# Kernel optimization log

Measured on AMD Instinct MI355X. Metric: run time of the kernel, lower is better.

Reference implementation:

```python
import jax, jax.numpy as jnp
import numpy as np

D_MODEL = 512
STATE_DIM = 32
ACTION_DIM = 8
D_STATE = 16
D_CONV = 4
EXPAND = 2
D_INNER = EXPAND * D_MODEL          # 1024
DT_RANK = (D_MODEL + 15) // 16      # 32
BATCH, SEQLEN = 16, 1024


def silu(v):
    return v * jax.nn.sigmoid(v)


def setup_inputs() -> dict:
    key = jax.random.key(0)
    ks = jax.random.split(key, 16)
    s = 0.02
    inp = {
        "x": jax.random.normal(ks[0], (BATCH, SEQLEN, STATE_DIM), jnp.float32),
        "W_emb": jax.random.normal(ks[1], (D_MODEL, STATE_DIM), jnp.float32) * s,
        "b_emb": jnp.zeros((D_MODEL,), jnp.float32),
        "W_in": jax.random.normal(ks[2], (2 * D_INNER, D_MODEL), jnp.float32) * s,
        "conv_w": jax.random.normal(ks[3], (D_INNER, 1, D_CONV), jnp.float32) * s,
        "conv_b": jnp.zeros((D_INNER,), jnp.float32),
        "W_xproj": jax.random.normal(ks[4], (DT_RANK + 2 * D_STATE, D_INNER), jnp.float32) * s,
        "W_dt": jax.random.normal(ks[5], (D_INNER, DT_RANK), jnp.float32) * s,
        "b_dt": jnp.full((D_INNER,), -4.6, jnp.float32),  # ~softplus^-1(0.01)
        "A_log": jnp.log(jnp.broadcast_to(
            jnp.arange(1, D_STATE + 1, dtype=jnp.float32), (D_INNER, D_STATE))),
        "Dskip": jnp.ones((D_INNER,), jnp.float32),
        "W_out": jax.random.normal(ks[6], (D_MODEL, D_INNER), jnp.float32) * s,
        "W_critic": jax.random.normal(ks[7], (1, D_MODEL), jnp.float32) * s,
        "b_critic": jnp.zeros((1,), jnp.float32),
        "W_amean": jax.random.normal(ks[8], (ACTION_DIM, D_MODEL), jnp.float32) * 0.01,  # orthogonal gain=0.01 proxy
        "b_amean": jnp.zeros((ACTION_DIM,), jnp.float32),
        "W_astd": jax.random.normal(ks[9], (ACTION_DIM, D_MODEL), jnp.float32) * s,
        "b_astd": jnp.zeros((ACTION_DIM,), jnp.float32),
    }
    return inp


def _forward(x, W_emb, b_emb, W_in, conv_w, conv_b, W_xproj, W_dt, b_dt,
             A_log, Dskip, W_out, W_critic, b_critic, W_amean, b_amean,
             W_astd, b_astd):
    Bsz = x.shape[0]
    embed = silu(x @ W_emb.T + b_emb)                      # (B,L,D)
    xz = embed @ W_in.T                                     # (B,L,2*Di)
    xu, z = jnp.split(xz, 2, axis=-1)
    # depthwise causal conv1d over time
    xc = jnp.transpose(xu, (0, 2, 1))                       # (B,Di,L)
    conv = jax.lax.conv_general_dilated(
        xc, conv_w, window_strides=(1,), padding=[(D_CONV - 1, 0)],
        dimension_numbers=("NCH", "OIH", "NCH"),
        feature_group_count=D_INNER) + conv_b[None, :, None]
    u = silu(jnp.transpose(conv, (0, 2, 1)))                # (B,L,Di)
    x_dbl = u @ W_xproj.T                                   # (B,L,dt_rank+2N)
    dt, Bm, Cm = jnp.split(x_dbl, [DT_RANK, DT_RANK + D_STATE], axis=-1)
    delta = jax.nn.softplus(dt @ W_dt.T + b_dt)             # (B,L,Di)
    A = -jnp.exp(A_log)                                     # (Di,N)

    # selective scan, time-major
    dlt = jnp.transpose(delta, (1, 0, 2))
    ut = jnp.transpose(u, (1, 0, 2))
    Bt = jnp.transpose(Bm, (1, 0, 2))
    Ct = jnp.transpose(Cm, (1, 0, 2))

    def step(h, inps):
        d_t, u_t, b_t, c_t = inps                           # (B,Di),(B,Di),(B,N),(B,N)
        dA = jnp.exp(d_t[..., None] * A)                    # (B,Di,N)
        h = dA * h + (d_t * u_t)[..., None] * b_t[:, None, :]
        y = jnp.einsum("bdn,bn->bd", h, c_t)
        return h, y

    h0 = jnp.zeros((Bsz, D_INNER, D_STATE), embed.dtype)
    _, ys = jax.lax.scan(step, h0, (dlt, ut, Bt, Ct))       # ys: (L,B,Di)
    y = jnp.transpose(ys, (1, 0, 2)) + u * Dskip
    y = y * silu(z)
    m = y @ W_out.T                                         # (B,L,D)

    # layer_norm (no affine) + silu, last token
    mu = m.mean(-1, keepdims=True)
    var = ((m - mu) ** 2).mean(-1, keepdims=True)
    n = silu((m - mu) / jnp.sqrt(var + 1e-5))[:, -1]        # (B,D)

    value = (n @ W_critic.T + b_critic).squeeze(-1)         # (B,)
    action_mean = n @ W_amean.T + b_amean                   # (B,A)
    log_std = jnp.clip(n @ W_astd.T + b_astd, -1.0, 1.0)
    action_sd = jnp.exp(log_std)
    return action_mean, action_sd, value


def reference(x, W_emb, b_emb, W_in, conv_w, conv_b, W_xproj, W_dt, b_dt,
              A_log, Dskip, W_out, W_critic, b_critic, W_amean, b_amean,
              W_astd, b_astd):
    # Returns the Normal distribution parameters (mean, std) and value,
    # matching torch's (Normal(mean, sd), value).
    return _forward(x, W_emb, b_emb, W_in, conv_w, conv_b, W_xproj, W_dt,
                    b_dt, A_log, Dskip, W_out, W_critic, b_critic,
                    W_amean, b_amean, W_astd, b_astd)
```

## Files before the change

### kernel.cpp

```cpp
#include <hip/hip_runtime.h>
#include <hip/hip_bf16.h>
#include <math.h>

#define B_   16
#define L_   1024
#define DM   512
#define DI   1024
#define NST  16
#define DTR  32
#define ML   (B_*L_)
#define SEGT 64
#define NSEG (L_/SEGT)

typedef __hip_bfloat16 bf16;
typedef __attribute__((ext_vector_type(8))) short short8;
typedef __attribute__((ext_vector_type(4))) float f32x4;

__device__ __forceinline__ float bf2f(unsigned short u) {
  union { unsigned int i; float f; } v; v.i = ((unsigned int)u) << 16; return v.f;
}
__device__ __forceinline__ unsigned short f2bfbits(float f) {
  bf16 h = __float2bfloat16(f);
  return *(unsigned short*)&h;
}
__device__ __forceinline__ float sigmoidf_(float v) { return 1.f/(1.f+__expf(-v)); }
__device__ __forceinline__ float ldf(const void* p, size_t i, int fl) {
  return fl ? bf2f(((const unsigned short*)p)[i]) : ((const float*)p)[i];
}
__device__ __forceinline__ void gload16(const void* g, void* l) {
  __builtin_amdgcn_global_load_lds(
      (const __attribute__((address_space(1))) void*)g,
      (__attribute__((address_space(3))) void*)l, 16, 0, 0);
}
__device__ __forceinline__ short8 ds_read128(unsigned addr) {
  short8 r;
  asm volatile("ds_read_b128 %0, %1" : "=v"(r) : "v"(addr));
  return r;
}

template<typename T> struct LD8;
template<> struct LD8<unsigned short> {
  static __device__ __forceinline__ short8 ld(const void* p, size_t i) {
    return *(const short8*)((const unsigned short*)p + i);
  }
  static __device__ __forceinline__ float lds(const void* p, size_t i) {
    return bf2f(((const unsigned short*)p)[i]);
  }
};
template<> struct LD8<float> {
  static __device__ __forceinline__ short8 ld(const void* p, size_t i) {
    const float* fp = (const float*)p + i;
    float4 f0 = *(const float4*)fp;
    float4 f1 = *(const float4*)(fp + 4);
    short8 v;
    v[0]=(short)f2bfbits(f0.x); v[1]=(short)f2bfbits(f0.y);
    v[2]=(short)f2bfbits(f0.z); v[3]=(short)f2bfbits(f0.w);
    v[4]=(short)f2bfbits(f1.x); v[5]=(short)f2bfbits(f1.y);
    v[6]=(short)f2bfbits(f1.z); v[7]=(short)f2bfbits(f1.w);
    return v;
  }
  static __device__ __forceinline__ float lds(const void* p, size_t i) {
    return ((const float*)p)[i];
  }
};

__global__ void detect_k(const unsigned int* __restrict__ x,
                         const void* __restrict__ A_log, int* __restrict__ flag) {
  int tid = threadIdx.x;
  int cnt = 0;
  for (int i = tid; i < 256; i += 64) {
    float a = fabsf(bf2f((unsigned short)(x[i] & 0xffffu)));
    if (a > 1e-3f && a < 10.f) cnt++;
  }
  for (int off = 32; off >= 1; off >>= 1) cnt += __shfl_xor(cnt, off);
  int fl = (cnt >= 128) ? 1 : 0;
  int n = tid & 15;
  int row = (tid < 16) ? 0 : (tid < 32 ? 512 : 1023);
  float al = ldf(A_log, (size_t)row*NST + n, fl);
  int ok = (fabsf(al - __logf((float)(n+1))) <= 0.02f) ? 1 : 0;
  for (int off = 32; off >= 1; off >>= 1) ok &= __shfl_xor(ok, off);
  if (tid == 0) { flag[0] = fl; flag[1] = ok; flag[2] = 1; }
}

__global__ __launch_bounds__(256) void convert_k(
    const void* __restrict__ x, const void* __restrict__ W_emb,
    const void* __restrict__ b_emb, const void* __restrict__ W_in,
    const void* __restrict__ W_xproj,
    unsigned short* __restrict__ xbf, unsigned short* __restrict__ webf,
    unsigned short* __restrict__ bebf, unsigned short* __restrict__ wibf,
    unsigned short* __restrict__ wxbf, const int* __restrict__ flag)
{
  const int fl = *flag;
  size_t t = (size_t)blockIdx.x*256 + threadIdx.x;
  const size_t n0 = (size_t)ML*32/8;
  const size_t n1 = (size_t)DM*32/8;
  const size_t n2 = DM/8;
  const size_t n3 = (size_t)DI*DM/8;
  const size_t n4 = (size_t)64*DI/8;
  const void* src; unsigned short* dst; size_t e;
  if      (t < n0)             { src = x;       dst = xbf;  e = t; }
  else if (t < n0+n1)          { src = W_emb;   dst = webf; e = t-n0; }
  else if (t < n0+n1+n2)       { src = b_emb;   dst = bebf; e = t-n0-n1; }
  else if (t < n0+n1+n2+n3)    { src = W_in;    dst = wibf; e = t-n0-n1-n2; }
  else if (t < n0+n1+n2+n3+n4) { src = W_xproj; dst = wxbf; e = t-n0-n1-n2-n3; }
  else return;
  size_t i = e*8;
  if (fl) *(short8*)&dst[i] = *(const short8*)((const unsigned short*)src + i);
  else    *(short8*)&dst[i] = LD8<float>::ld(src, i);
}

__global__ __launch_bounds__(512, 2) void gemm256_k(
    const unsigned short* __restrict__ A, const unsigned short* __restrict__ W,
    unsigned short* __restrict__ C, int K, int lda, int ldb, int ldc,
    const void* __restrict__ conv_w, const void* __restrict__ conv_b,
    unsigned short* __restrict__ xubnd, const int* __restrict__ flag)
{
  if (!flag[2]) return;
  __shared__ unsigned short smem[2][2][256*64];
  const int tid = threadIdx.x;
  const int lane = tid & 63;
  const int wv = tid >> 6;
  const int wr = wv >> 2;
  const int wc = wv & 3;
  const int m0 = blockIdx.x * 256;
  const int n0 = blockIdx.y * 256;
  const int lr = lane & 15, lg = lane >> 4;
  const int drow = lane >> 3;
  const int scol = ((lane & 7) ^ drow) * 8;
  const int NKT = K >> 6;
  const unsigned lds0 = (unsigned)(unsigned long long)
      (__attribute__((address_space(3))) void*)&smem[0][0][0];

  f32x4 acc[8][4];
  #pragma unroll
  for (int i = 0; i < 8; ++i)
    #pragma unroll
    for (int j = 0; j < 4; ++j) acc[i][j] = (f32x4){0.f, 0.f, 0.f, 0.f};

  auto stage = [&](int buf, int kt) {
    #pragma unroll
    for (int q = 0; q < 4; ++q) {
      int rb = (wv*4 + q) * 8;
      gload16(A + (size_t)(m0 + rb + drow)*lda + kt*64 + scol, &smem[buf][0][rb*64]);
    }
    #pragma unroll
    for (int q = 0; q < 4; ++q) {
      int rb = (wv*4 + q) * 8;
      gload16(W + (size_t)(n0 + rb + drow)*ldb + kt*64 + scol, &smem[buf][1][rb*64]);
    }
  };

  stage(0, 0);
  stage(1, 1);
  for (int kt = 0; kt < NKT; ++kt) {
    int buf = kt & 1;
    if (kt + 1 < NKT) asm volatile("s_waitcnt vmcnt(8)" ::: "memory");
    else              asm volatile("s_waitcnt vmcnt(0)" ::: "memory");
    __builtin_amdgcn_s_barrier();
    __builtin_amdgcn_sched_barrier(0);
    const unsigned aBase = lds0 + (unsigned)(buf*2 + 0)*(256*64*2);
    const unsigned bBase = lds0 + (unsigned)(buf*2 + 1)*(256*64*2);
    #pragma unroll
    for (int kk = 0; kk < 64; kk += 32) {
      const int ukk = (((kk >> 3) + lg) ^ (lr & 7)) * 8;
      short8 af[8], bfr[4];
      #pragma unroll
      for (int i = 0; i < 8; ++i)
        af[i] = ds_read128(aBase + (unsigned)(((wr*128 + i*16 + lr)*64 + ukk)*2));
      #pragma unroll
      for (int j = 0; j < 4; ++j)
        bfr[j] = ds_read128(bBase + (unsigned)(((wc*64 + j*16 + lr)*64 + ukk)*2));
      asm volatile("s_waitcnt lgkmcnt(0)" ::: "memory");
      __builtin_amdgcn_sched_barrier(0);
      __builtin_amdgcn_s_setprio(1);
      #pragma unroll
      for (int i = 0; i < 8; ++i)
        #pragma unroll
        for (int j = 0; j < 4; ++j)
          acc[i][j] = __builtin_amdgcn_mfma_f32_16x16x32_bf16(af[i], bfr[j], acc[i][j], 0, 0, 0);
      __builtin_amdgcn_s_setprio(0);
    }
    __builtin_amdgcn_s_barrier();
    __builtin_amdgcn_sched_barrier(0);
    if (kt + 2 < NKT) stage(buf, kt + 2);
  }

  unsigned short* cs = (unsigned short*)smem;
  #pragma unroll
  for (int j = 0; j < 4; ++j) {
    int c = wc*64 + j*16 + lr;
    #pragma unroll
    for (int i = 0; i < 8; ++i) {
      int rbase = wr*128 + i*16 + lg*4;
      #pragma unroll
      for (int r = 0; r < 4; ++r)
        cs[(rbase + r)*256 + c] = f2bfbits(acc[i][j][r]);
    }
  }
  __syncthreads();
  const int fl = flag[0];
  const int t0loc = m0 & (L_ - 1);
  const int colb = (tid & 31) * 8;
  const int rowbase = (tid >> 5) * 16;
  float wt[8][4], bt[8];
  #pragma unroll
  for (int e = 0; e < 8; ++e) {
    int d = n0 + colb + e;
    #pragma unroll
    for (int q = 0; q < 4; ++q) wt[e][q] = ldf(conv_w, (size_t)d*4 + q, fl);
    bt[e] = ldf(conv_b, d, fl);
  }
  const int tileIdx = blockIdx.x*4 + blockIdx.y;
  short8 zer;
  #pragma unroll
  for (int e = 0; e < 8; ++e) zer[e] = 0;
  short8 c1 = (rowbase >= 1) ? *(const short8*)&cs[(rowbase-1)*256 + colb] : zer;
  short8 c2 = (rowbase >= 2) ? *(const short8*)&cs[(rowbase-2)*256 + colb] : zer;
  short8 c3 = (rowbase >= 3) ? *(const short8*)&cs[(rowbase-3)*256 + colb] : zer;
  #pragma unroll
  for (int k = 0; k < 16; ++k) {
    int row = rowbase + k;
    short8 c0 = *(const short8*)&cs[row*256 + colb];
    if (row < 3 || row >= 253) {
      int rm = (row < 3) ? row : row - 250;
      *(short8*)&xubnd[((size_t)tileIdx*6 + rm)*256 + colb] = c0;
    }
    if (!(row < 3 && t0loc != 0)) {
      short8 out;
      #pragma unroll
      for (int e = 0; e < 8; ++e) {
        float ca  = bf2f((unsigned short)c0[e]);
        float am1 = bf2f((unsigned short)c1[e]);
        float am2 = bf2f((unsigned short)c2[e]);
        float am3 = bf2f((unsigned short)c3[e]);
        float va = wt[e][0]*am3 + wt[e][1]*am2 + wt[e][2]*am1 + wt[e][3]*ca + bt[e];
        va = va * sigmoidf_(va);
        out[e] = (short)f2bfbits(va);
      }
      *(short8*)&C[(size_t)(m0 + row)*ldc + n0 + colb] = out;
    }
    c3 = c2; c2 = c1; c1 = c0;
  }
}

__global__ __launch_bounds__(256) void convfix_k(
    const unsigned short* __restrict__ xubnd,
    const void* __restrict__ conv_w, const void* __restrict__ conv_b,
    unsigned short* __restrict__ u, const int* __restrict__ flag)
{
  int tile = blockIdx.x;
  int r = blockIdx.y;
  int mt = tile >> 2, nt = tile & 3;
  int m0 = mt*256, n0 = nt*256;
  if ((m0 & (L_ - 1)) == 0) return;
  int col = threadIdx.x;
  int d = n0 + col;
  int fl = flag[0];
  float vin[4];
  #pragma unroll
  for (int q = 0; q < 4; ++q) {
    int trow = r - 3 + q;
    int stile, srm;
    if (trow < 0) { stile = tile - 4; srm = 6 + trow; }
    else          { stile = tile;     srm = trow; }
    vin[q] = bf2f(xubnd[((size_t)stile*6 + srm)*256 + col]);
  }
  float w0 = ldf(conv_w, (size_t)d*4 + 0, fl);
  float w1 = ldf(conv_w, (size_t)d*4 + 1, fl);
  float w2 = ldf(conv_w, (size_t)d*4 + 2, fl);
  float w3 = ldf(conv_w, (size_t)d*4 + 3, fl);
  float bb = ldf(conv_b, d, fl);
  float va = w0*vin[0] + w1*vin[1] + w2*vin[2] + w3*vin[3] + bb;
  va = va * sigmoidf_(va);
  u[(size_t)(m0 + r)*DI + d] = f2bfbits(va);
}


template<int BM, int BN, int BK>
__device__ __forceinline__ void mfma_body_dma(
    const unsigned short* __restrict__ A, const unsigned short* __restrict__ W,
    const unsigned short* __restrict__ bias, void* __restrict__ Cv,
    int K, int lda, int ldb, int ldc, int mode, size_t csplit)
{
  extern __shared__ unsigned short smem[];
  unsigned short* As = smem;
  unsigned short* Bs = smem + BM*BK;
  constexpr int MIM = (BM == 64) ? 4 : ((BN == 128) ? 4 : 2);
  constexpr int MIN = (BM == 64) ? 2 : 4;
  constexpr int RPI = 1024/(2*BK);
  constexpr int LPR = 64/RPI;
  const int tid = threadIdx.x;
  const int m0 = blockIdx.x * BM;
  const int n0 = blockIdx.y * BN;
  const int kbase = blockIdx.z * K;
  const int lane = tid & 63;
  const int wv = tid >> 6;
  const int wm = (BM == 64) ? 0 : ((BN == 128) ? (wv >> 1) * 64 : wv * 32);
  const int wn = (BM == 64) ? wv * 32 : ((BN == 128) ? (wv & 1) * 64 : 0);
  const int lr = lane & 15, lg = lane >> 4;
  const int drow = lane / LPR;
  const int dcol = (lane % LPR) * 8;

  f32x4 acc[MIM][MIN];
  #pragma unroll
  for (int i = 0; i < MIM; ++i)
    #pragma unroll
    for (int j = 0; j < MIN; ++j) acc[i][j] = (f32x4){0.f, 0.f, 0.f, 0.f};

  for (int k0 = 0; k0 < K; k0 += BK) {
    __syncthreads();
    #pragma unroll
    for (int q = 0; q < BM/RPI/4; ++q) {
      int rb = (wv*(BM/RPI/4) + q) * RPI;
      gload16(A + (size_t)(m0 + rb + drow)*lda + kbase + k0 + dcol, &As[rb*BK]);
    }
    #pragma unroll
    for (int q = 0; q < BN/RPI/4; ++q) {
      int rb = (wv*(BN/RPI/4) + q) * RPI;
      gload16(W + (size_t)(n0 + rb + drow)*ldb + kbase + k0 + dcol, &Bs[rb*BK]);
    }
    __syncthreads();
    #pragma unroll
    for (int kk = 0; kk < BK; kk += 32) {
      short8 af[MIM], bfr[MIN];
      #pragma unroll
      for (int i = 0; i < MIM; ++i)
        af[i] = *(const short8*)&As[(wm + i*16 + lr)*BK + kk + lg*8];
      #pragma unroll
      for (int j = 0; j < MIN; ++j)
        bfr[j] = *(const short8*)&Bs[(wn + j*16 + lr)*BK + kk + lg*8];
      #pragma unroll
      for (int i = 0; i < MIM; ++i)
        #pragma unroll
        for (int j = 0; j < MIN; ++j)
          acc[i][j] = __builtin_amdgcn_mfma_f32_16x16x32_bf16(af[i], bfr[j], acc[i][j], 0, 0, 0);
    }
  }

  size_t cz = (size_t)blockIdx.z * csplit;
  #pragma unroll
  for (int j = 0; j < MIN; ++j) {
    int gn = n0 + wn + j*16 + lr;
    float bv = (mode == 1) ? bf2f(bias[gn]) : 0.f;
    #pragma unroll
    for (int i = 0; i < MIM; ++i) {
      #pragma unroll
      for (int r = 0; r < 4; ++r) {
        int gm = m0 + wm + i*16 + lg*4 + r;
        float v = acc[i][j][r];
        if (mode == 1) {
          v += bv; v = v * sigmoidf_(v);
          ((unsigned short*)Cv)[cz + (size_t)gm*ldc + gn] = f2bfbits(v);
        } else if (mode == 3) {
          ((unsigned short*)Cv)[cz + (size_t)gm*ldc + gn] = f2bfbits(v);
        } else {
          ((float*)Cv)[cz + (size_t)gm*ldc + gn] = v;
        }
      }
    }
  }
}

template<typename TA, typename TW, int BM, int BN>
__device__ __forceinline__ void mfma_body(
    const void* __restrict__ Av, const void* __restrict__ Wv,
    const void* __restrict__ biasv, void* __restrict__ Cv,
    int K, int lda, int ldb, int ldc, int mode, size_t csplit)
{
  extern __shared__ unsigned short smem[];
  unsigned short* As = smem;
  unsigned short* Bs = smem + BM*40;
  constexpr int MIM = (BM == 64) ? 4 : ((BN == 128) ? 4 : 2);
  constexpr int MIN = (BM == 64) ? 2 : 4;
  const int tid = threadIdx.x;
  const int m0 = blockIdx.x * BM;
  const int n0 = blockIdx.y * BN;
  const int kbase = blockIdx.z * K;
  const int lane = tid & 63;
  const int wv = tid >> 6;
  const int wm = (BM == 64) ? 0 : ((BN == 128) ? (wv >> 1) * 64 : wv * 32);
  const int wn = (BM == 64) ? wv * 32 : ((BN == 128) ? (wv & 1) * 64 : 0);
  const int lr = lane & 15, lg = lane >> 4;

  f32x4 acc[MIM][MIN];
  #pragma unroll
  for (int i = 0; i < MIM; ++i)
    #pragma unroll
    for (int j = 0; j < MIN; ++j) acc[i][j] = (f32x4){0.f, 0.f, 0.f, 0.f};

  for (int k0 = 0; k0 < K; k0 += 32) {
    short8 ra[BM/64], rb[BN/64];
    #pragma unroll
    for (int r = 0; r < BM/64; ++r) {
      int chunk = tid + r*256;
      int row = chunk >> 2, sub = (chunk & 3) * 8;
      ra[r] = LD8<TA>::ld(Av, (size_t)(m0 + row)*lda + kbase + k0 + sub);
    }
    #pragma unroll
    for (int r = 0; r < BN/64; ++r) {
      int chunk = tid + r*256;
      int row = chunk >> 2, sub = (chunk & 3) * 8;
      rb[r] = LD8<TW>::ld(Wv, (size_t)(n0 + row)*ldb + kbase + k0 + sub);
    }
    __syncthreads();
    #pragma unroll
    for (int r = 0; r < BM/64; ++r) {
      int chunk = tid + r*256;
      int row = chunk >> 2, sub = (chunk & 3) * 8;
      *(short8*)&As[row*40 + sub] = ra[r];
    }
    #pragma unroll
    for (int r = 0; r < BN/64; ++r) {
      int chunk = tid + r*256;
      int row = chunk >> 2, sub = (chunk & 3) * 8;
      *(short8*)&Bs[row*40 + sub] = rb[r];
    }
    __syncthreads();
    short8 af[MIM], bfr[MIN];
    #pragma unroll
    for (int i = 0; i < MIM; ++i)
      af[i] = *(const short8*)&As[(wm + i*16 + lr)*40 + lg*8];
    #pragma unroll
    for (int j = 0; j < MIN; ++j)
      bfr[j] = *(const short8*)&Bs[(wn + j*16 + lr)*40 + lg*8];
    #pragma unroll
    for (int i = 0; i < MIM; ++i)
      #pragma unroll
      for (int j = 0; j < MIN; ++j)
        acc[i][j] = __builtin_amdgcn_mfma_f32_16x16x32_bf16(af[i], bfr[j], acc[i][j], 0, 0, 0);
  }

  size_t cz = (size_t)blockIdx.z * csplit;
  #pragma unroll
  for (int j = 0; j < MIN; ++j) {
    int gn = n0 + wn + j*16 + lr;
    float bv = (mode == 1) ? LD8<TW>::lds(biasv, gn) : 0.f;
    #pragma unroll
    for (int i = 0; i < MIM; ++i) {
      #pragma unroll
      for (int r = 0; r < 4; ++r) {
        int gm = m0 + wm + i*16 + lg*4 + r;
        float v = acc[i][j][r];
        if (mode == 1) {
          v += bv; v = v * sigmoidf_(v);
          ((unsigned short*)Cv)[cz + (size_t)gm*ldc + gn] = f2bfbits(v);
        } else if (mode == 3) {
          ((unsigned short*)Cv)[cz + (size_t)gm*ldc + gn] = f2bfbits(v);
        } else {
          ((float*)Cv)[cz + (size_t)gm*ldc + gn] = v;
        }
      }
    }
  }
}

template<int BM, int BN, int BK>
__global__ __launch_bounds__(256) void gemm_a16_k(const void* A, const void* W,
    const void* bias, void* C, int K, int lda, int ldb, int ldc, int mode,
    size_t csplit, const int* __restrict__ flag)
{
  if (*flag) mfma_body_dma<BM, BN, BK>((const unsigned short*)A, (const unsigned short*)W,
                                       (const unsigned short*)bias, C, K, lda, ldb, ldc, mode, csplit);
  else       mfma_body<unsigned short, float, BM, BN>(A, W, bias, C, K, lda, ldb, ldc, mode, csplit);
}

__global__ __launch_bounds__(256) void dt_gemm_k(
    const float* __restrict__ xd, const void* __restrict__ W_dt,
    const void* __restrict__ b_dt, unsigned short* __restrict__ delta,
    const int* __restrict__ flag)
{
  __shared__ unsigned short As[128*40];
  __shared__ unsigned short Bs[128*40];
  const int tid = threadIdx.x;
  const int m0 = blockIdx.x * 128;
  const int n0 = blockIdx.y * 128;
  const int fl = *flag;
  const int row = tid >> 1, half = (tid & 1) * 16;
  {
    size_t g = (size_t)(m0 + row)*64 + half;
    const float* p0 = xd + g;
    const float* p1 = xd + (size_t)ML*64 + g;
    short8 v0, v1;
    #pragma unroll
    for (int q = 0; q < 8; q += 4) {
      float4 a4 = *(const float4*)(p0 + q);
      float4 b4 = *(const float4*)(p1 + q);
      v0[q+0] = (short)f2bfbits(a4.x + b4.x);
      v0[q+1] = (short)f2bfbits(a4.y + b4.y);
      v0[q+2] = (short)f2bfbits(a4.z + b4.z);
      v0[q+3] = (short)f2bfbits(a4.w + b4.w);
    }
    #pragma unroll
    for (int q = 0; q < 8; q += 4) {
      float4 a4 = *(const float4*)(p0 + 8 + q);
      float4 b4 = *(const float4*)(p1 + 8 + q);
      v1[q+0] = (short)f2bfbits(a4.x + b4.x);
      v1[q+1] = (short)f2bfbits(a4.y + b4.y);
      v1[q+2] = (short)f2bfbits(a4.z + b4.z);
      v1[q+3] = (short)f2bfbits(a4.w + b4.w);
    }
    *(short8*)&As[row*40 + half] = v0;
    *(short8*)&As[row*40 + half + 8] = v1;
  }
  {
    *(short8*)&Bs[row*40 + half]     = fl ? LD8<unsigned short>::ld(W_dt, (size_t)(n0+row)*DTR + half)
                                          : LD8<float>::ld(W_dt, (size_t)(n0+row)*DTR + half);
    *(short8*)&Bs[row*40 + half + 8] = fl ? LD8<unsigned short>::ld(W_dt, (size_t)(n0+row)*DTR + half + 8)
                                          : LD8<float>::ld(W_dt, (size_t)(n0+row)*DTR + half + 8);
  }
  __syncthreads();
  const int lane = tid & 63;
  const int wv = tid >> 6;
  const int wm = (wv >> 1) * 64, wn = (wv & 1) * 64;
  const int lr = lane & 15, lg = lane >> 4;
  f32x4 acc[4][4];
  #pragma unroll
  for (int i = 0; i < 4; ++i)
    #pragma unroll
    for (int j = 0; j < 4; ++j) acc[i][j] = (f32x4){0.f, 0.f, 0.f, 0.f};
  short8 af[4], bfr[4];
  #pragma unroll
  for (int i = 0; i < 4; ++i)
    af[i] = *(const short8*)&As[(wm + i*16 + lr)*40 + lg*8];
  #pragma unroll
  for (int j = 0; j < 4; ++j)
    bfr[j] = *(const short8*)&Bs[(wn + j*16 + lr)*40 + lg*8];
  #pragma unroll
  for (int i = 0; i < 4; ++i)
    #pragma unroll
    for (int j = 0; j < 4; ++j)
      acc[i][j] = __builtin_amdgcn_mfma_f32_16x16x32_bf16(af[i], bfr[j], acc[i][j], 0, 0, 0);
  #pragma unroll
  for (int j = 0; j < 4; ++j) {
    int gn = n0 + wn + j*16 + lr;
    float bv = ldf(b_dt, gn, fl);
    #pragma unroll
    for (int i = 0; i < 4; ++i) {
      #pragma unroll
      for (int r = 0; r < 4; ++r) {
        int gm = m0 + wm + i*16 + lg*4 + r;
        float v = acc[i][j][r] + bv;
        v = (v > 20.f) ? v : __logf(1.f + __expf(v));
        delta[(size_t)gm*DI + gn] = f2bfbits(v);
      }
    }
  }
}

__global__ __launch_bounds__(256) void zlast2_k(const unsigned short* __restrict__ embed,
    const void* __restrict__ W_in, float* __restrict__ z_last, const int* __restrict__ flag)
{
  int b = blockIdx.x;
  int j0 = blockIdx.y * 64;
  int tid = threadIdx.x;
  __shared__ float e[DM];
  for (int i = tid; i < DM; i += 256)
    e[i] = bf2f(embed[(size_t)(b*L_ + L_-1)*DM + i]);
  __syncthreads();
  int fl = *flag;
  int wid = tid >> 6, lane = tid & 63;
  for (int jj = wid; jj < 64; jj += 4) {
    int j = j0 + jj;
    float p = 0.f;
    int k = lane * 8;
    if (fl) {
      const unsigned short* w = (const unsigned short*)W_in + (size_t)(DI + j)*DM + k;
      short8 v = *(const short8*)w;
      #pragma unroll
      for (int q = 0; q < 8; ++q) p += e[k+q]*bf2f((unsigned short)v[q]);
    } else {
      const float* w = (const float*)W_in + (size_t)(DI + j)*DM + k;
      float4 v0 = *(const float4*)w;
      float4 v1 = *(const float4*)(w + 4);
      p = e[k]*v0.x + e[k+1]*v0.y + e[k+2]*v0.z + e[k+3]*v0.w
        + e[k+4]*v1.x + e[k+5]*v1.y + e[k+6]*v1.z + e[k+7]*v1.w;
    }
    for (int off = 32; off >= 1; off >>= 1) p += __shfl_xor(p, off);
    if (lane == 0) z_last[b*DI + j] = p;
  }
}

__global__ __launch_bounds__(256) void scan4_k(
    const unsigned short* __restrict__ delta, const unsigned short* __restrict__ u,
    const float* __restrict__ xd, const void* __restrict__ A_log,
    unsigned int* __restrict__ ps, const int* __restrict__ flag)
{
  const int b = blockIdx.x;
  const int d0 = blockIdx.y * 256;
  const int seg = blockIdx.z;
  const int t0 = seg * SEGT;
  const int tid = threadIdx.x;
  const int d = d0 + tid;
  const int fl = flag[0];
  const int fast = flag[1];
  __shared__ float sB[SEGT*16];
  #pragma unroll
  for (int i = 0; i < SEGT*16/256; ++i) {
    int idx = tid + i*256;
    int row = idx >> 4, n = idx & 15;
    size_t g = (size_t)(b*L_ + t0 + row)*64 + 32 + n;
    sB[idx] = xd[g] + xd[(size_t)ML*64 + g];
  }
  float h[16];
  #pragma unroll
  for (int n = 0; n < 16; ++n) h[n] = 0.f;
  float sdt = 0.f;
  const unsigned short* dp = delta + (size_t)(b*L_ + t0)*DI + d;
  const unsigned short* up = u + (size_t)(b*L_ + t0)*DI + d;
  __syncthreads();
  if (fast) {
    unsigned short nd = dp[0], nu = up[0];
    for (int t = 0; t < SEGT; ++t) {
      float dt = bf2f(nd), ut = bf2f(nu);
      if (t < SEGT-1) { nd = dp[(size_t)(t+1)*DI]; nu = up[(size_t)(t+1)*DI]; }
      float g = dt * ut;
      sdt += dt;
      const float* Br = &sB[t*16];
      float e1 = __expf(-dt);
      float e = e1;
      h[0] = e*h[0] + g*Br[0];
      #pragma unroll
      for (int n = 1; n < 16; ++n) {
        e *= e1;
        h[n] = e*h[n] + g*Br[n];
      }
    }
    float E1 = __expf(-sdt);
    float P = 1.f;
    #pragma unroll
    for (int n = 0; n < 16; ++n) {
      P *= E1;
      ps[(((size_t)seg*16 + b)*16 + n)*DI + d] =
          ((unsigned int)f2bfbits(h[n]) << 16) | f2bfbits(P);
    }
  } else {
    float a[16];
    #pragma unroll
    for (int n = 0; n < 16; ++n)
      a[n] = -__expf(ldf(A_log, (size_t)d*NST + n, fl));
    unsigned short nd = dp[0], nu = up[0];
    for (int t = 0; t < SEGT; ++t) {
      float dt = bf2f(nd), ut = bf2f(nu);
      if (t < SEGT-1) { nd = dp[(size_t)(t+1)*DI]; nu = up[(size_t)(t+1)*DI]; }
      float g = dt * ut;
      sdt += dt;
      const float* Br = &sB[t*16];
      #pragma unroll
      for (int n = 0; n < 16; ++n)
        h[n] = __expf(dt*a[n])*h[n] + g*Br[n];
    }
    #pragma unroll
    for (int n = 0; n < 16; ++n)
      ps[(((size_t)seg*16 + b)*16 + n)*DI + d] =
          ((unsigned int)f2bfbits(h[n]) << 16) | f2bfbits(__expf(a[n]*sdt));
  }
}

__global__ __launch_bounds__(256) void combine4_k(const unsigned int* __restrict__ ps,
    const float* __restrict__ xd, float* __restrict__ ypart)
{
  int b = blockIdx.x;
  int d = blockIdx.y * 256 + threadIdx.x;
  int n0 = blockIdx.z * 4;
  float h[4] = {0.f, 0.f, 0.f, 0.f};
  for (int s = 0; s < NSEG; ++s) {
    #pragma unroll
    for (int q = 0; q < 4; ++q) {
      unsigned int v = ps[(((size_t)s*16 + b)*16 + n0 + q)*DI + d];
      h[q] = bf2f((unsigned short)v)*h[q] + bf2f((unsigned short)(v >> 16));
    }
  }
  float y = 0.f;
  #pragma unroll
  for (int q = 0; q < 4; ++q) {
    size_t gl = (size_t)(b*L_ + L_-1)*64 + 48 + n0 + q;
    float cn = xd[gl] + xd[(size_t)ML*64 + gl];
    y += h[q]*cn;
  }
  ypart[((size_t)blockIdx.z*16 + b)*DI + d] = y;
}

__global__ __launch_bounds__(256) void mdot_k(const float* __restrict__ ypart,
    const unsigned short* __restrict__ u, const float* __restrict__ z_last,
    const void* __restrict__ Dskip, const void* __restrict__ W_out,
    float* __restrict__ m_out, const int* __restrict__ flag)
{
  int b = blockIdx.x;
  int r0 = blockIdx.y * 64;
  int tid = threadIdx.x;
  const int fl = *flag;
  __shared__ float yz[DI];
  for (int i = tid; i < DI; i += 256) {
    float ys = ypart[(size_t)b*DI + i] + ypart[(size_t)(16+b)*DI + i]
             + ypart[(size_t)(32+b)*DI + i] + ypart[(size_t)(48+b)*DI + i]
             + bf2f(u[(size_t)(b*L_ + L_-1)*DI + i]) * ldf(Dskip, i, fl);
    float z = z_last[b*DI + i];
    yz[i] = ys * (z * sigmoidf_(z));
  }
  __syncthreads();
  int wid = tid >> 6, lane = tid & 63;
  int k = lane * 8;
  for (int rr = wid; rr < 64; rr += 4) {
    int row = r0 + rr;
    float p = 0.f;
    if (fl) {
      const unsigned short* w = (const unsigned short*)W_out + (size_t)row*DI;
      short8 v0 = *(const short8*)(w + k);
      short8 v1 = *(const short8*)(w + 512 + k);
      #pragma unroll
      for (int q = 0; q < 8; ++q)
        p += yz[k+q]*bf2f((unsigned short)v0[q]) + yz[512+k+q]*bf2f((unsigned short)v1[q]);
    } else {
      const float* w = (const float*)W_out + (size_t)row*DI;
      float4 a0 = *(const float4*)(w + k),      a1 = *(const float4*)(w + k + 4);
      float4 b0 = *(const float4*)(w + 512 + k), b1 = *(const float4*)(w + 512 + k + 4);
      p = yz[k]*a0.x + yz[k+1]*a0.y + yz[k+2]*a0.z + yz[k+3]*a0.w
        + yz[k+4]*a1.x + yz[k+5]*a1.y + yz[k+6]*a1.z + yz[k+7]*a1.w
        + yz[512+k]*b0.x + yz[512+k+1]*b0.y + yz[512+k+2]*b0.z + yz[512+k+3]*b0.w
        + yz[512+k+4]*b1.x + yz[512+k+5]*b1.y + yz[512+k+6]*b1.z + yz[512+k+7]*b1.w;
    }
    for (int off = 32; off >= 1; off >>= 1) p += __shfl_xor(p, off);
    if (lane == 0) m_out[b*DM + row] = p;
  }
}

__global__ __launch_bounds__(512) void head2_k(const float* __restrict__ m_in,
    const void* __restrict__ W_critic, const void* __restrict__ b_critic,
    const void* __restrict__ W_amean, const void* __restrict__ b_amean,
    const void* __restrict__ W_astd, const void* __restrict__ b_astd,
    void* __restrict__ out, const int* __restrict__ flag)
{
  __shared__ float nb[DM];
  __shared__ float w1[8], w2[8];
  const int fl = *flag;
  int b = blockIdx.x;
  int tid = threadIdx.x;
  float m = m_in[b*DM + tid];
  float s1 = m, s2 = m*m;
  for (int off = 32; off >= 1; off >>= 1) { s1 += __shfl_xor(s1, off); s2 += __shfl_xor(s2, off); }
  int wid = tid >> 6, lane = tid & 63;
  if (lane == 0) { w1[wid] = s1; w2[wid] = s2; }
  __syncthreads();
  float t1 = 0.f, t2 = 0.f;
  for (int i = 0; i < 8; ++i) { t1 += w1[i]; t2 += w2[i]; }
  float mu  = t1 * (1.f/DM);
  float var = t2 * (1.f/DM) - mu*mu;
  float v = (m - mu) * rsqrtf(var + 1e-5f);
  nb[tid] = v * sigmoidf_(v);
  __syncthreads();
  for (int o = wid; o < 17; o += 8) {
    const void* w; size_t woff; float bias;
    if (o < 8)       { w = W_amean; woff = (size_t)o*DM;     bias = ldf(b_amean, o, fl); }
    else if (o < 16) { w = W_astd;  woff = (size_t)(o-8)*DM; bias = ldf(b_astd, o-8, fl); }
    else             { w = W_critic; woff = 0;               bias = ldf(b_critic, 0, fl); }
    float p = 0.f;
    for (int j = lane; j < DM; j += 64) p += nb[j] * ldf(w, woff + j, fl);
    for (int off = 32; off >= 1; off >>= 1) p += __shfl_xor(p, off);
    if (lane == 0) {
      float r = p + bias;
      int idx; float val;
      if (o < 8)       { idx = b*8 + o;           val = r; }
      else if (o < 16) { float ls = fminf(1.f, fmaxf(-1.f, r));
                         idx = 128 + b*8 + (o-8); val = expf(ls); }
      else             { idx = 256 + b;           val = r; }
      if (fl) ((bf16*)out)[idx] = __float2bfloat16(val);
      else    ((float*)out)[idx] = val;
    }
  }
}

extern "C" void kernel_launch(void* const* d_in, const int* in_sizes, int n_in,
                              void* d_out, int out_size, void* d_ws, size_t ws_size,
                              hipStream_t stream)
{
  const void* x        = d_in[0];
  const void* W_emb    = d_in[1];
  const void* b_emb    = d_in[2];
  const void* W_in     = d_in[3];
  const void* conv_w   = d_in[4];
  const void* conv_b   = d_in[5];
  const void* W_xproj  = d_in[6];
  const void* W_dt     = d_in[7];
  const void* b_dt     = d_in[8];
  const void* A_log    = d_in[9];
  const void* Dskip    = d_in[10];
  const void* W_out    = d_in[11];
  const void* W_critic = d_in[12];
  const void* b_critic = d_in[13];
  const void* W_amean  = d_in[14];
  const void* b_amean  = d_in[15];
  const void* W_astd   = d_in[16];
  const void* b_astd   = d_in[17];

  char* ws = (char*)d_ws;
  unsigned short* embed_bf = (unsigned short*)ws; ws += (size_t)ML*DM*2;
  unsigned short* dlt_b = (unsigned short*)ws; ws += (size_t)ML*DI*2;
  unsigned short* u_b   = (unsigned short*)ws; ws += (size_t)ML*DI*2;
  float* xdbl2 = (float*)ws; ws += (size_t)2*ML*64*4;
  unsigned int* psbuf = (unsigned int*)ws; ws += (size_t)NSEG*B_*NST*DI*4;
  float* ypart = (float*)ws; ws += (size_t)4*B_*DI*4;
  float* zlast = (float*)ws; ws += (size_t)B_*DI*4;
  float* mbuf  = (float*)ws; ws += (size_t)B_*DM*4;
  int*   flag  = (int*)ws;   ws += 64;
  unsigned short* xbf  = (unsigned short*)ws; ws += (size_t)ML*32*2;
  unsigned short* webf = (unsigned short*)ws; ws += (size_t)DM*32*2;
  unsigned short* bebf = (unsigned short*)ws; ws += (size_t)DM*2;
  unsigned short* wibf = (unsigned short*)ws; ws += (size_t)DI*DM*2;
  unsigned short* wxbf = (unsigned short*)ws; ws += (size_t)64*DI*2;
  unsigned short* xubnd = (unsigned short*)ws; ws += (size_t)256*6*256*2;
  const int* flagBF = flag + 2;

  detect_k<<<1, 64, 0, stream>>>((const unsigned int*)x, A_log, flag);
  convert_k<<<553, 256, 0, stream>>>(x, W_emb, b_emb, W_in, W_xproj,
                                     xbf, webf, bebf, wibf, wxbf, flag);
  gemm_a16_k<128, 128, 32><<<dim3(ML/128, DM/128), 256, 256*40*2, stream>>>(
      xbf, webf, bebf, embed_bf, 32, 32, 32, DM, 1, 0, flagBF);
  gemm256_k<<<dim3(ML/256, DI/256), 512, 0, stream>>>(
      embed_bf, wibf, u_b, DM, DM, DM, DI, conv_w, conv_b, xubnd, flag);
  convfix_k<<<dim3(256, 3), 256, 0, stream>>>(xubnd, conv_w, conv_b, u_b, flag);
  zlast2_k<<<dim3(16, 16), 256, 0, stream>>>(embed_bf, W_in, zlast, flag);
  gemm_a16_k<128, 64, 64><<<dim3(ML/128, 1, 2), 256, 24576, stream>>>(
      u_b, wxbf, nullptr, xdbl2, 512, DI, DI, 64, 0, (size_t)ML*64, flagBF);
  dt_gemm_k<<<dim3(ML/128, DI/128), 256, 0, stream>>>(
      xdbl2, W_dt, b_dt, dlt_b, flag);
  scan4_k<<<dim3(B_, 4, NSEG), 256, 0, stream>>>(
      dlt_b, u_b, xdbl2, A_log, psbuf, flag);
  combine4_k<<<dim3(B_, 4, 4), 256, 0, stream>>>(psbuf, xdbl2, ypart);
  mdot_k<<<dim3(16, 8), 256, 0, stream>>>(ypart, u_b, zlast, Dskip, W_out, mbuf, flag);
  head2_k<<<16, 512, 0, stream>>>(mbuf, W_critic, b_critic,
                                  W_amean, b_amean, W_astd, b_astd, (void*)d_out, flag);
}
```

Baseline: 251.0 us.

## Fuse dt projection GEMM and softplus into the segmented scan kernel

Removes the separate dt_gemm kernel and computes delta for each scan segment inside the scan kernel. The kernel uses one MFMA per 16x16 tile from the dt-rank slice of xdbl and a bf16 copy of W_dt, applies softplus, and stores the result in shared memory. This avoids writing and re-reading a B*L*DI bf16 delta tensor in global memory and saves one launch. In exchange, the scan kernel uses more shared memory, does extra prologue work per block, and takes on a convert_k pass that converts W_dt to bf16.

```diff
diff --git a/kernel.cpp b/kernel.cpp
--- a/kernel.cpp
+++ b/kernel.cpp
@@ -85,10 +85,11 @@
 __global__ __launch_bounds__(256) void convert_k(
     const void* __restrict__ x, const void* __restrict__ W_emb,
     const void* __restrict__ b_emb, const void* __restrict__ W_in,
-    const void* __restrict__ W_xproj,
+    const void* __restrict__ W_xproj, const void* __restrict__ W_dt,
     unsigned short* __restrict__ xbf, unsigned short* __restrict__ webf,
     unsigned short* __restrict__ bebf, unsigned short* __restrict__ wibf,
-    unsigned short* __restrict__ wxbf, const int* __restrict__ flag)
+    unsigned short* __restrict__ wxbf, unsigned short* __restrict__ wdtbf,
+    const int* __restrict__ flag)
 {
   const int fl = *flag;
   size_t t = (size_t)blockIdx.x*256 + threadIdx.x;
@@ -97,12 +98,14 @@
   const size_t n2 = DM/8;
   const size_t n3 = (size_t)DI*DM/8;
   const size_t n4 = (size_t)64*DI/8;
+  const size_t n5 = (size_t)DI*DTR/8;
   const void* src; unsigned short* dst; size_t e;
-  if      (t < n0)             { src = x;       dst = xbf;  e = t; }
-  else if (t < n0+n1)          { src = W_emb;   dst = webf; e = t-n0; }
-  else if (t < n0+n1+n2)       { src = b_emb;   dst = bebf; e = t-n0-n1; }
-  else if (t < n0+n1+n2+n3)    { src = W_in;    dst = wibf; e = t-n0-n1-n2; }
-  else if (t < n0+n1+n2+n3+n4) { src = W_xproj; dst = wxbf; e = t-n0-n1-n2-n3; }
+  if      (t < n0)                { src = x;       dst = xbf;   e = t; }
+  else if (t < n0+n1)             { src = W_emb;   dst = webf;  e = t-n0; }
+  else if (t < n0+n1+n2)          { src = b_emb;   dst = bebf;  e = t-n0-n1; }
+  else if (t < n0+n1+n2+n3)       { src = W_in;    dst = wibf;  e = t-n0-n1-n2; }
+  else if (t < n0+n1+n2+n3+n4)    { src = W_xproj; dst = wxbf;  e = t-n0-n1-n2-n3; }
+  else if (t < n0+n1+n2+n3+n4+n5) { src = W_dt;    dst = wdtbf; e = t-n0-n1-n2-n3-n4; }
   else return;
   size_t i = e*8;
   if (fl) *(short8*)&dst[i] = *(const short8*)((const unsigned short*)src + i);
@@ -464,89 +467,6 @@
   else       mfma_body<unsigned short, float, BM, BN>(A, W, bias, C, K, lda, ldb, ldc, mode, csplit);
 }
 
-__global__ __launch_bounds__(256) void dt_gemm_k(
-    const float* __restrict__ xd, const void* __restrict__ W_dt,
-    const void* __restrict__ b_dt, unsigned short* __restrict__ delta,
-    const int* __restrict__ flag)
-{
-  __shared__ unsigned short As[128*40];
-  __shared__ unsigned short Bs[128*40];
-  const int tid = threadIdx.x;
-  const int m0 = blockIdx.x * 128;
-  const int n0 = blockIdx.y * 128;
-  const int fl = *flag;
-  const int row = tid >> 1, half = (tid & 1) * 16;
-  {
-    size_t g = (size_t)(m0 + row)*64 + half;
-    const float* p0 = xd + g;
-    const float* p1 = xd + (size_t)ML*64 + g;
-    short8 v0, v1;
-    #pragma unroll
-    for (int q = 0; q < 8; q += 4) {
-      float4 a4 = *(const float4*)(p0 + q);
-      float4 b4 = *(const float4*)(p1 + q);
-      v0[q+0] = (short)f2bfbits(a4.x + b4.x);
-      v0[q+1] = (short)f2bfbits(a4.y + b4.y);
-      v0[q+2] = (short)f2bfbits(a4.z + b4.z);
-      v0[q+3] = (short)f2bfbits(a4.w + b4.w);
-    }
-    #pragma unroll
-    for (int q = 0; q < 8; q += 4) {
-      float4 a4 = *(const float4*)(p0 + 8 + q);
-      float4 b4 = *(const float4*)(p1 + 8 + q);
-      v1[q+0] = (short)f2bfbits(a4.x + b4.x);
-      v1[q+1] = (short)f2bfbits(a4.y + b4.y);
-      v1[q+2] = (short)f2bfbits(a4.z + b4.z);
-      v1[q+3] = (short)f2bfbits(a4.w + b4.w);
-    }
-    *(short8*)&As[row*40 + half] = v0;
-    *(short8*)&As[row*40 + half + 8] = v1;
-  }
-  {
-    *(short8*)&Bs[row*40 + half]     = fl ? LD8<unsigned short>::ld(W_dt, (size_t)(n0+row)*DTR + half)
-                                          : LD8<float>::ld(W_dt, (size_t)(n0+row)*DTR + half);
-    *(short8*)&Bs[row*40 + half + 8] = fl ? LD8<unsigned short>::ld(W_dt, (size_t)(n0+row)*DTR + half + 8)
-                                          : LD8<float>::ld(W_dt, (size_t)(n0+row)*DTR + half + 8);
-  }
-  __syncthreads();
-  const int lane = tid & 63;
-  const int wv = tid >> 6;
-  const int wm = (wv >> 1) * 64, wn = (wv & 1) * 64;
-  const int lr = lane & 15, lg = lane >> 4;
-  f32x4 acc[4][4];
-  #pragma unroll
-  for (int i = 0; i < 4; ++i)
-    #pragma unroll
-    for (int j = 0; j < 4; ++j) acc[i][j] = (f32x4){0.f, 0.f, 0.f, 0.f};
-  short8 af[4], bfr[4];
-  #pragma unroll
-  for (int i = 0; i < 4; ++i)
-    af[i] = *(const short8*)&As[(wm + i*16 + lr)*40 + lg*8];
-  #pragma unroll
-  for (int j = 0; j < 4; ++j)
-    bfr[j] = *(const short8*)&Bs[(wn + j*16 + lr)*40 + lg*8];
-  #pragma unroll
-  for (int i = 0; i < 4; ++i)
-    #pragma unroll
-    for (int j = 0; j < 4; ++j)
-      acc[i][j] = __builtin_amdgcn_mfma_f32_16x16x32_bf16(af[i], bfr[j], acc[i][j], 0, 0, 0);
-  #pragma unroll
-  for (int j = 0; j < 4; ++j) {
-    int gn = n0 + wn + j*16 + lr;
-    float bv = ldf(b_dt, gn, fl);
-    #pragma unroll
-    for (int i = 0; i < 4; ++i) {
-      #pragma unroll
-      for (int r = 0; r < 4; ++r) {
-        int gm = m0 + wm + i*16 + lg*4 + r;
-        float v = acc[i][j][r] + bv;
-        v = (v > 20.f) ? v : __logf(1.f + __expf(v));
-        delta[(size_t)gm*DI + gn] = f2bfbits(v);
-      }
-    }
-  }
-}
-
 __global__ __launch_bounds__(256) void zlast2_k(const unsigned short* __restrict__ embed,
     const void* __restrict__ W_in, float* __restrict__ z_last, const int* __restrict__ flag)
 {
@@ -580,10 +500,11 @@
   }
 }
 
-__global__ __launch_bounds__(256) void scan4_k(
-    const unsigned short* __restrict__ delta, const unsigned short* __restrict__ u,
-    const float* __restrict__ xd, const void* __restrict__ A_log,
-    unsigned int* __restrict__ ps, const int* __restrict__ flag)
+__global__ __launch_bounds__(256) void scan6_k(
+    const unsigned short* __restrict__ u, const float* __restrict__ xd,
+    const unsigned short* __restrict__ wdtbf, const void* __restrict__ b_dt,
+    const void* __restrict__ A_log, unsigned int* __restrict__ ps,
+    const int* __restrict__ flag)
 {
   const int b = blockIdx.x;
   const int d0 = blockIdx.y * 256;
@@ -594,6 +515,8 @@
   const int fl = flag[0];
   const int fast = flag[1];
   __shared__ float sB[SEGT*16];
+  __shared__ unsigned short sDT[SEGT*32];
+  __shared__ unsigned short sDelta[SEGT*256];
   #pragma unroll
   for (int i = 0; i < SEGT*16/256; ++i) {
     int idx = tid + i*256;
@@ -601,18 +524,43 @@
     size_t g = (size_t)(b*L_ + t0 + row)*64 + 32 + n;
     sB[idx] = xd[g] + xd[(size_t)ML*64 + g];
   }
+  #pragma unroll
+  for (int i = 0; i < SEGT*32/256; ++i) {
+    int idx = tid + i*256;
+    size_t g = (size_t)(b*L_ + t0 + (idx >> 5))*64 + (idx & 31);
+    sDT[idx] = f2bfbits(xd[g] + xd[(size_t)ML*64 + g]);
+  }
+  __syncthreads();
+  {
+    const int lane = tid & 63;
+    const int wv4 = tid >> 6;
+    const int lr = lane & 15, lg = lane >> 4;
+    short8 af = *(const short8*)&sDT[(wv4*16 + lr)*32 + lg*8];
+    #pragma unroll
+    for (int j = 0; j < 16; ++j) {
+      short8 bfr = *(const short8*)&wdtbf[(size_t)(d0 + j*16 + lr)*DTR + lg*8];
+      f32x4 a4 = (f32x4){0.f, 0.f, 0.f, 0.f};
+      a4 = __builtin_amdgcn_mfma_f32_16x16x32_bf16(af, bfr, a4, 0, 0, 0);
+      float bv = ldf(b_dt, d0 + j*16 + lr, fl);
+      #pragma unroll
+      for (int r = 0; r < 4; ++r) {
+        float v = a4[r] + bv;
+        v = (v > 20.f) ? v : __logf(1.f + __expf(v));
+        sDelta[(wv4*16 + lg*4 + r)*256 + j*16 + lr] = f2bfbits(v);
+      }
+    }
+  }
   float h[16];
   #pragma unroll
   for (int n = 0; n < 16; ++n) h[n] = 0.f;
   float sdt = 0.f;
-  const unsigned short* dp = delta + (size_t)(b*L_ + t0)*DI + d;
   const unsigned short* up = u + (size_t)(b*L_ + t0)*DI + d;
   __syncthreads();
   if (fast) {
-    unsigned short nd = dp[0], nu = up[0];
+    unsigned short nu = up[0];
     for (int t = 0; t < SEGT; ++t) {
-      float dt = bf2f(nd), ut = bf2f(nu);
-      if (t < SEGT-1) { nd = dp[(size_t)(t+1)*DI]; nu = up[(size_t)(t+1)*DI]; }
+      float dt = bf2f(sDelta[t*256 + tid]), ut = bf2f(nu);
+      if (t < SEGT-1) nu = up[(size_t)(t+1)*DI];
       float g = dt * ut;
       sdt += dt;
       const float* Br = &sB[t*16];
@@ -638,10 +586,10 @@
     #pragma unroll
     for (int n = 0; n < 16; ++n)
       a[n] = -__expf(ldf(A_log, (size_t)d*NST + n, fl));
-    unsigned short nd = dp[0], nu = up[0];
+    unsigned short nu = up[0];
     for (int t = 0; t < SEGT; ++t) {
-      float dt = bf2f(nd), ut = bf2f(nu);
-      if (t < SEGT-1) { nd = dp[(size_t)(t+1)*DI]; nu = up[(size_t)(t+1)*DI]; }
+      float dt = bf2f(sDelta[t*256 + tid]), ut = bf2f(nu);
+      if (t < SEGT-1) nu = up[(size_t)(t+1)*DI];
       float g = dt * ut;
       sdt += dt;
       const float* Br = &sB[t*16];
@@ -794,7 +742,6 @@
 
   char* ws = (char*)d_ws;
   unsigned short* embed_bf = (unsigned short*)ws; ws += (size_t)ML*DM*2;
-  unsigned short* dlt_b = (unsigned short*)ws; ws += (size_t)ML*DI*2;
   unsigned short* u_b   = (unsigned short*)ws; ws += (size_t)ML*DI*2;
   float* xdbl2 = (float*)ws; ws += (size_t)2*ML*64*4;
   unsigned int* psbuf = (unsigned int*)ws; ws += (size_t)NSEG*B_*NST*DI*4;
@@ -807,12 +754,13 @@
   unsigned short* bebf = (unsigned short*)ws; ws += (size_t)DM*2;
   unsigned short* wibf = (unsigned short*)ws; ws += (size_t)DI*DM*2;
   unsigned short* wxbf = (unsigned short*)ws; ws += (size_t)64*DI*2;
+  unsigned short* wdtbf = (unsigned short*)ws; ws += (size_t)DI*DTR*2;
   unsigned short* xubnd = (unsigned short*)ws; ws += (size_t)256*6*256*2;
   const int* flagBF = flag + 2;
 
   detect_k<<<1, 64, 0, stream>>>((const unsigned int*)x, A_log, flag);
-  convert_k<<<553, 256, 0, stream>>>(x, W_emb, b_emb, W_in, W_xproj,
-                                     xbf, webf, bebf, wibf, wxbf, flag);
+  convert_k<<<569, 256, 0, stream>>>(x, W_emb, b_emb, W_in, W_xproj, W_dt,
+                                     xbf, webf, bebf, wibf, wxbf, wdtbf, flag);
   gemm_a16_k<128, 128, 32><<<dim3(ML/128, DM/128), 256, 256*40*2, stream>>>(
       xbf, webf, bebf, embed_bf, 32, 32, 32, DM, 1, 0, flagBF);
   gemm256_k<<<dim3(ML/256, DI/256), 512, 0, stream>>>(
@@ -821,10 +769,8 @@
   zlast2_k<<<dim3(16, 16), 256, 0, stream>>>(embed_bf, W_in, zlast, flag);
   gemm_a16_k<128, 64, 64><<<dim3(ML/128, 1, 2), 256, 24576, stream>>>(
       u_b, wxbf, nullptr, xdbl2, 512, DI, DI, 64, 0, (size_t)ML*64, flagBF);
-  dt_gemm_k<<<dim3(ML/128, DI/128), 256, 0, stream>>>(
-      xdbl2, W_dt, b_dt, dlt_b, flag);
-  scan4_k<<<dim3(B_, 4, NSEG), 256, 0, stream>>>(
-      dlt_b, u_b, xdbl2, A_log, psbuf, flag);
+  scan6_k<<<dim3(B_, 4, NSEG), 256, 0, stream>>>(
+      u_b, xdbl2, wdtbf, b_dt, A_log, psbuf, flag);
   combine4_k<<<dim3(B_, 4, 4), 256, 0, stream>>>(psbuf, xdbl2, ypart);
   mdot_k<<<dim3(16, 8), 256, 0, stream>>>(ypart, u_b, zlast, Dskip, W_out, mbuf, flag);
   head2_k<<<16, 512, 0, stream>>>(mbuf, W_critic, b_critic,
```

Measured after the change: 248.4 us, median of 2. About the same (-1.0%).
